# Optimization experiments

Measured on AMD Instinct MI355X. Metric: run time of the kernel, lower is better.

Reference implementation:

```python
import jax, jax.numpy as jnp
import numpy as np

NEG_BIG = -9e15
ALPHA = 0.1  # leaky relu slope


def setup_inputs() -> dict:
    key = jax.random.key(0)
    k1, k2, k3, k4 = jax.random.split(key, 4)
    B, C, N, F = 4, 4, 2048, 64
    x = jax.random.normal(k1, (B, C, N, F), dtype=jnp.float32)
    adj = jax.random.randint(k2, (N, N), 0, 2, dtype=jnp.int32)
    # xavier_uniform on shape (1,1,F,1): fan_in=1, fan_out=F -> bound = 1.414*sqrt(6/(1+F))
    bound = 1.414 * np.sqrt(6.0 / (1.0 + F))
    a1 = jax.random.uniform(k3, (F, 1), jnp.float32, -bound, bound)
    a2 = jax.random.uniform(k4, (F, 1), jnp.float32, -bound, bound)
    return {"x": x, "adj": adj, "a1": a1, "a2": a2}


def reference(x, adj, a1, a2):
    # x: [B, C, N, F]; adj: [N, N]; a1, a2: [F, 1]
    h = x
    f1 = jnp.einsum("bcnf,fo->bcn", h, a1)  # [B, C, N]
    f2 = jnp.einsum("bcnf,fo->bcn", h, a2)  # [B, C, N]
    e = f1[..., :, None] + f2[..., None, :]  # [B, C, N, N] additive scores
    e = jnp.where(e > 0, e, ALPHA * e)       # leaky relu
    e = jnp.where(adj[None, None] > 0, e, jnp.float32(NEG_BIG))
    attention = jax.nn.softmax(e, axis=-1)
    # dropout is identity in eval mode (training=False)
    return jnp.matmul(attention, h)          # [B, C, N, F]
```

## Files before the change

### kernel.cpp

```cpp
#include <hip/hip_runtime.h>
#include <hip/hip_bf16.h>
#include <cstdint>

#define NN 2048
#define FF 64
#define BCC 16

typedef float f32x4 __attribute__((ext_vector_type(4)));
typedef _Float16 half8 __attribute__((ext_vector_type(8)));
typedef uint32_t u32x4 __attribute__((ext_vector_type(4)));


__global__ __launch_bounds__(256) void k_prep(const float* __restrict__ x,
        const int* __restrict__ adj,
        const float* __restrict__ a1, const float* __restrict__ a2,
        _Float16* __restrict__ xP, _Float16* __restrict__ Uh,
        _Float16* __restrict__ Vh, _Float16* __restrict__ CIh,
        unsigned char* __restrict__ ADJP) {
    int tid = threadIdx.x;

    if (blockIdx.x >= 1024) {
        int wid  = tid >> 6;
        int lane = tid & 63;
        int idx = (blockIdx.x - 1024) * 4 + wid;
        int row = idx >> 3, cg = idx & 7;
        const int* p = adj + (size_t)row * NN + cg * 256 + lane;
        unsigned long long m0 = __ballot(p[0]   > 0);
        unsigned long long m1 = __ballot(p[64]  > 0);
        unsigned long long m2 = __ballot(p[128] > 0);
        unsigned long long m3 = __ballot(p[192] > 0);
        if (lane < 32) {
            int q = lane >> 3, s = lane & 7;
            unsigned long long m = (q == 0) ? m0 : (q == 1) ? m1
                                 : (q == 2) ? m2 : m3;
            unsigned char byte = (unsigned char)(m >> (8 * s));
            int jt = (cg * 4 + q) * 2 + (s >> 2);
            int g  = s & 3;
            ADJP[(size_t)row * 256 + g * 64 + jt] = byte;
        }
        return;
    }

    __shared__ float tile[32][65];
    __shared__ float red[2][32][8];
    int bc = blockIdx.x >> 6;
    int n0 = (blockIdx.x & 63) * 32;
    int row = tid >> 3;
    int fo  = (tid & 7) * 8;

    const float* xr = x + ((size_t)bc * NN + n0 + row) * FF + fo;
    f32x4 v0 = *(const f32x4*)xr;
    f32x4 v1 = *(const f32x4*)(xr + 4);
    *(f32x4*)&tile[row][fo]     = v0;
    *(f32x4*)&tile[row][fo + 4] = v1;

    f32x4 a1v0 = *(const f32x4*)(a1 + fo);
    f32x4 a1v1 = *(const f32x4*)(a1 + fo + 4);
    f32x4 a2v0 = *(const f32x4*)(a2 + fo);
    f32x4 a2v1 = *(const f32x4*)(a2 + fo + 4);
    float d1 = 0.f, d2 = 0.f;
    #pragma unroll
    for (int e = 0; e < 4; e++) {
        d1 += v0[e] * a1v0[e] + v1[e] * a1v1[e];
        d2 += v0[e] * a2v0[e] + v1[e] * a2v1[e];
    }
    red[0][row][tid & 7] = d1;
    red[1][row][tid & 7] = d2;
    __syncthreads();

    {
        int nb = tid >> 6, lane = tid & 63;
        int g = lane >> 4, l15 = lane & 15;
        half8 val;
        #pragma unroll
        for (int e = 0; e < 8; e++)
            val[e] = (_Float16)tile[8 * g + e][nb * 16 + l15];
        ((half8*)xP)[(((size_t)bc * 64 + (n0 >> 5)) * 4 + nb) * 64 + lane] = val;
    }
    if (tid < 32) {
        float f1 = 0.f, f2 = 0.f;
        #pragma unroll
        for (int s = 0; s < 8; s++) { f1 += red[0][tid][s]; f2 += red[1][tid][s]; }
        int idx = bc * NN + n0 + tid;
        Uh[idx]  = (_Float16)expf(f2);
        Vh[idx]  = (_Float16)expf(0.1f * f2);
        CIh[idx] = (_Float16)expf(-0.9f * f1);
    }
}

__global__ __launch_bounds__(256) void k_main(
        const _Float16* __restrict__ xP, const _Float16* __restrict__ Uh,
        const _Float16* __restrict__ Vh, const _Float16* __restrict__ CIh,
        const unsigned char* __restrict__ ADJP, float* __restrict__ out) {
    __shared__ _Float16 su[2048];
    __shared__ _Float16 sv[2048];
    __shared__ u32x4 lut[256];
    __shared__ float part[4][16][68];
    __shared__ float zp[4][16];

    int tid = threadIdx.x;
    int jq = tid >> 6, lane = tid & 63;
    int l15 = lane & 15, g = lane >> 4;

    int xcd = blockIdx.x & 7, kk = blockIdx.x >> 3;
    int bc   = (xcd << 1) | (kk >> 5);
    int iblk = kk & 31;
    int i0   = iblk * 64;

    ((u32x4*)su)[tid] = ((const u32x4*)(Uh + bc * NN))[tid];
    ((u32x4*)sv)[tid] = ((const u32x4*)(Vh + bc * NN))[tid];
    {
        uint32_t bb = tid;
        u32x4 lv;
        #pragma unroll
        for (int w = 0; w < 4; w++)
            lv[w] = (((bb >> (2 * w)) & 1u) ? 0xFFFFu : 0u)
                  | (((bb >> (2 * w + 1)) & 1u) ? 0xFFFF0000u : 0u);
        lut[bb] = lv;
    }
    const unsigned char* ab = ADJP + g * 64 + jq * 16;
    u32x4 adjw0 = *(const u32x4*)(ab + (size_t)(i0 + l15) * 256);
    u32x4 adjw1 = *(const u32x4*)(ab + (size_t)(i0 + 16 + l15) * 256);
    u32x4 adjw2 = *(const u32x4*)(ab + (size_t)(i0 + 32 + l15) * 256);
    u32x4 adjw3 = *(const u32x4*)(ab + (size_t)(i0 + 48 + l15) * 256);
    _Float16 Ci0 = CIh[bc * NN + i0 + l15];
    _Float16 Ci1 = CIh[bc * NN + i0 + 16 + l15];
    _Float16 Ci2 = CIh[bc * NN + i0 + 32 + l15];
    _Float16 Ci3 = CIh[bc * NN + i0 + 48 + l15];
    __syncthreads();

    f32x4 acc[4][4];
    #pragma unroll
    for (int a = 0; a < 4; a++)
        #pragma unroll
        for (int nb = 0; nb < 4; nb++)
            acc[a][nb] = (f32x4){0.f, 0.f, 0.f, 0.f};
    f32x4 accz[4];
    #pragma unroll
    for (int a = 0; a < 4; a++) accz[a] = (f32x4){0.f, 0.f, 0.f, 0.f};
    half8 onesh;
    #pragma unroll
    for (int e = 0; e < 8; e++) onesh[e] = (_Float16)1.0f;

    const u32x4* xPbc = (const u32x4*)xP + (size_t)bc * 16384;

    u32x4 A_x0, A_x1, A_x2, A_x3, B_x0, B_x1, B_x2, B_x3;

#define LOADX(P, J) do {                                                      \
        const u32x4* xw_ = xPbc + (((size_t)(jq * 16 + (J))) << 8) + lane;    \
        P##x0 = xw_[0]; P##x1 = xw_[64]; P##x2 = xw_[128]; P##x3 = xw_[192];  \
    } while (0)

#define GEN(AF, ADJW, CI) do {                                                \
        uint32_t b_ = (ADJW[(J_) >> 2] >> (((J_) & 3) * 8)) & 0xffu;          \
        u32x4 mm_ = lut[b_];                                                  \
        half8 mx_ = __builtin_elementwise_max(uu_, vv_ * (CI));               \
        AF = __builtin_bit_cast(half8, __builtin_bit_cast(u32x4, mx_) & mm_); \
    } while (0)

#define COMP(P, J) do {                                                       \
        const int J_ = (J);                                                   \
        const int jo_ = (jq * 16 + J_) * 32 + 8 * g;                          \
        half8 uu_ = *(const half8*)&su[jo_];                                  \
        half8 vv_ = *(const half8*)&sv[jo_];                                  \
        half8 af0_, af1_, af2_, af3_;                                         \
        GEN(af0_, adjw0, Ci0); GEN(af1_, adjw1, Ci1);                         \
        GEN(af2_, adjw2, Ci2); GEN(af3_, adjw3, Ci3);                         \
        half8 b0_ = __builtin_bit_cast(half8, P##x0);                         \
        half8 b1_ = __builtin_bit_cast(half8, P##x1);                         \
        half8 b2_ = __builtin_bit_cast(half8, P##x2);                         \
        half8 b3_ = __builtin_bit_cast(half8, P##x3);                         \
        __builtin_amdgcn_s_setprio(1);                                        \
        acc[0][0] = __builtin_amdgcn_mfma_f32_16x16x32_f16(af0_, b0_, acc[0][0], 0, 0, 0); \
        acc[0][1] = __builtin_amdgcn_mfma_f32_16x16x32_f16(af0_, b1_, acc[0][1], 0, 0, 0); \
        acc[0][2] = __builtin_amdgcn_mfma_f32_16x16x32_f16(af0_, b2_, acc[0][2], 0, 0, 0); \
        acc[0][3] = __builtin_amdgcn_mfma_f32_16x16x32_f16(af0_, b3_, acc[0][3], 0, 0, 0); \
        accz[0]   = __builtin_amdgcn_mfma_f32_16x16x32_f16(af0_, onesh, accz[0], 0, 0, 0); \
        acc[1][0] = __builtin_amdgcn_mfma_f32_16x16x32_f16(af1_, b0_, acc[1][0], 0, 0, 0); \
        acc[1][1] = __builtin_amdgcn_mfma_f32_16x16x32_f16(af1_, b1_, acc[1][1], 0, 0, 0); \
        acc[1][2] = __builtin_amdgcn_mfma_f32_16x16x32_f16(af1_, b2_, acc[1][2], 0, 0, 0); \
        acc[1][3] = __builtin_amdgcn_mfma_f32_16x16x32_f16(af1_, b3_, acc[1][3], 0, 0, 0); \
        accz[1]   = __builtin_amdgcn_mfma_f32_16x16x32_f16(af1_, onesh, accz[1], 0, 0, 0); \
        acc[2][0] = __builtin_amdgcn_mfma_f32_16x16x32_f16(af2_, b0_, acc[2][0], 0, 0, 0); \
        acc[2][1] = __builtin_amdgcn_mfma_f32_16x16x32_f16(af2_, b1_, acc[2][1], 0, 0, 0); \
        acc[2][2] = __builtin_amdgcn_mfma_f32_16x16x32_f16(af2_, b2_, acc[2][2], 0, 0, 0); \
        acc[2][3] = __builtin_amdgcn_mfma_f32_16x16x32_f16(af2_, b3_, acc[2][3], 0, 0, 0); \
        accz[2]   = __builtin_amdgcn_mfma_f32_16x16x32_f16(af2_, onesh, accz[2], 0, 0, 0); \
        acc[3][0] = __builtin_amdgcn_mfma_f32_16x16x32_f16(af3_, b0_, acc[3][0], 0, 0, 0); \
        acc[3][1] = __builtin_amdgcn_mfma_f32_16x16x32_f16(af3_, b1_, acc[3][1], 0, 0, 0); \
        acc[3][2] = __builtin_amdgcn_mfma_f32_16x16x32_f16(af3_, b2_, acc[3][2], 0, 0, 0); \
        acc[3][3] = __builtin_amdgcn_mfma_f32_16x16x32_f16(af3_, b3_, acc[3][3], 0, 0, 0); \
        accz[3]   = __builtin_amdgcn_mfma_f32_16x16x32_f16(af3_, onesh, accz[3], 0, 0, 0); \
        __builtin_amdgcn_s_setprio(0);                                        \
    } while (0)

    LOADX(A_, 0);
    LOADX(B_, 1);  COMP(A_, 0);
    LOADX(A_, 2);  COMP(B_, 1);
    LOADX(B_, 3);  COMP(A_, 2);
    LOADX(A_, 4);  COMP(B_, 3);
    LOADX(B_, 5);  COMP(A_, 4);
    LOADX(A_, 6);  COMP(B_, 5);
    LOADX(B_, 7);  COMP(A_, 6);
    LOADX(A_, 8);  COMP(B_, 7);
    LOADX(B_, 9);  COMP(A_, 8);
    LOADX(A_, 10); COMP(B_, 9);
    LOADX(B_, 11); COMP(A_, 10);
    LOADX(A_, 12); COMP(B_, 11);
    LOADX(B_, 13); COMP(A_, 12);
    LOADX(A_, 14); COMP(B_, 13);
    LOADX(B_, 15); COMP(A_, 14);
    COMP(B_, 15);
#undef LOADX
#undef GEN
#undef COMP

    float* outp = out + ((size_t)bc * NN + i0) * FF;
    #pragma unroll
    for (int a = 0; a < 4; a++) {
        #pragma unroll
        for (int nb = 0; nb < 4; nb++)
            #pragma unroll
            for (int r = 0; r < 4; r++)
                part[jq][4 * g + r][nb * 16 + l15] = acc[a][nb][r];
        if (l15 == 0) {
            #pragma unroll
            for (int r = 0; r < 4; r++)
                zp[jq][4 * g + r] = accz[a][r];
        }
        __syncthreads();
        #pragma unroll
        for (int rr = 0; rr < 4; rr++) {
            int row = jq * 4 + rr;
            float s = part[0][row][lane] + part[1][row][lane]
                    + part[2][row][lane] + part[3][row][lane];
            float z = zp[0][row] + zp[1][row] + zp[2][row] + zp[3][row];
            outp[(size_t)(16 * a + row) * FF + lane] = s / z;
        }
        __syncthreads();
    }
}

extern "C" void kernel_launch(void* const* d_in, const int* in_sizes, int n_in,
                              void* d_out, int out_size, void* d_ws, size_t ws_size,
                              hipStream_t stream) {
    const float* x  = (const float*)d_in[0];
    const int* adj  = (const int*)d_in[1];
    const float* a1 = (const float*)d_in[2];
    const float* a2 = (const float*)d_in[3];
    float* out = (float*)d_out;

    char* ws = (char*)d_ws;
    _Float16* xP  = (_Float16*)ws;
    _Float16* Uh  = (_Float16*)(ws + 4194304);
    _Float16* Vh  = (_Float16*)(ws + 4259840);
    _Float16* CIh = (_Float16*)(ws + 4325376);
    unsigned char* ADJP = (unsigned char*)(ws + 4390912);

    k_prep<<<1024 + 4096, 256, 0, stream>>>(x, adj, a1, a2, xP, Uh, Vh, CIh, ADJP);
    k_main<<<512, 256, 0, stream>>>(xP, Uh, Vh, CIh, ADJP, out);
}
```

Baseline: 25.93 us.

## Merge prep work into 512 blocks and pack adjacency with vector loads

Shrinks the prep grid from thousands of blocks to 512. Each block now processes two x tiles and then packs four adjacency rows. Adjacency bits are built per thread from 16-byte vector loads instead of wave ballots, which cuts block-launch overhead and the instruction count per byte. The risk is less memory-level parallelism and latency hiding, since there are far fewer waves in flight on a bandwidth-bound prep stage.

```diff
diff --git a/kernel.cpp b/kernel.cpp
--- a/kernel.cpp
+++ b/kernel.cpp
@@ -7,6 +7,7 @@
 #define BCC 16
 
 typedef float f32x4 __attribute__((ext_vector_type(4)));
+typedef int   i32x4 __attribute__((ext_vector_type(4)));
 typedef _Float16 half8 __attribute__((ext_vector_type(8)));
 typedef uint32_t u32x4 __attribute__((ext_vector_type(4)));
 
@@ -17,74 +18,78 @@
         _Float16* __restrict__ xP, _Float16* __restrict__ Uh,
         _Float16* __restrict__ Vh, _Float16* __restrict__ CIh,
         unsigned char* __restrict__ ADJP) {
-    int tid = threadIdx.x;
-
-    if (blockIdx.x >= 1024) {
-        int wid  = tid >> 6;
-        int lane = tid & 63;
-        int idx = (blockIdx.x - 1024) * 4 + wid;
-        int row = idx >> 3, cg = idx & 7;
-        const int* p = adj + (size_t)row * NN + cg * 256 + lane;
-        unsigned long long m0 = __ballot(p[0]   > 0);
-        unsigned long long m1 = __ballot(p[64]  > 0);
-        unsigned long long m2 = __ballot(p[128] > 0);
-        unsigned long long m3 = __ballot(p[192] > 0);
-        if (lane < 32) {
-            int q = lane >> 3, s = lane & 7;
-            unsigned long long m = (q == 0) ? m0 : (q == 1) ? m1
-                                 : (q == 2) ? m2 : m3;
-            unsigned char byte = (unsigned char)(m >> (8 * s));
-            int jt = (cg * 4 + q) * 2 + (s >> 2);
-            int g  = s & 3;
-            ADJP[(size_t)row * 256 + g * 64 + jt] = byte;
-        }
-        return;
-    }
-
     __shared__ float tile[32][65];
     __shared__ float red[2][32][8];
-    int bc = blockIdx.x >> 6;
-    int n0 = (blockIdx.x & 63) * 32;
-    int row = tid >> 3;
-    int fo  = (tid & 7) * 8;
-
-    const float* xr = x + ((size_t)bc * NN + n0 + row) * FF + fo;
-    f32x4 v0 = *(const f32x4*)xr;
-    f32x4 v1 = *(const f32x4*)(xr + 4);
-    *(f32x4*)&tile[row][fo]     = v0;
-    *(f32x4*)&tile[row][fo + 4] = v1;
-
-    f32x4 a1v0 = *(const f32x4*)(a1 + fo);
-    f32x4 a1v1 = *(const f32x4*)(a1 + fo + 4);
-    f32x4 a2v0 = *(const f32x4*)(a2 + fo);
-    f32x4 a2v1 = *(const f32x4*)(a2 + fo + 4);
-    float d1 = 0.f, d2 = 0.f;
-    #pragma unroll
-    for (int e = 0; e < 4; e++) {
-        d1 += v0[e] * a1v0[e] + v1[e] * a1v1[e];
-        d2 += v0[e] * a2v0[e] + v1[e] * a2v1[e];
-    }
-    red[0][row][tid & 7] = d1;
-    red[1][row][tid & 7] = d2;
-    __syncthreads();
+    int tid = threadIdx.x;
+
+    #pragma unroll
+    for (int tt = 0; tt < 2; tt++) {
+        int t  = blockIdx.x * 2 + tt;
+        int bc = t >> 6;
+        int n0 = (t & 63) * 32;
+        int row = tid >> 3;
+        int fo  = (tid & 7) * 8;
+
+        const float* xr = x + ((size_t)bc * NN + n0 + row) * FF + fo;
+        f32x4 v0 = *(const f32x4*)xr;
+        f32x4 v1 = *(const f32x4*)(xr + 4);
+        *(f32x4*)&tile[row][fo]     = v0;
+        *(f32x4*)&tile[row][fo + 4] = v1;
+
+        f32x4 a1v0 = *(const f32x4*)(a1 + fo);
+        f32x4 a1v1 = *(const f32x4*)(a1 + fo + 4);
+        f32x4 a2v0 = *(const f32x4*)(a2 + fo);
+        f32x4 a2v1 = *(const f32x4*)(a2 + fo + 4);
+        float d1 = 0.f, d2 = 0.f;
+        #pragma unroll
+        for (int e = 0; e < 4; e++) {
+            d1 += v0[e] * a1v0[e] + v1[e] * a1v1[e];
+            d2 += v0[e] * a2v0[e] + v1[e] * a2v1[e];
+        }
+        red[0][row][tid & 7] = d1;
+        red[1][row][tid & 7] = d2;
+        __syncthreads();
+
+        {
+            int nb = tid >> 6, lane = tid & 63;
+            int g = lane >> 4, l15 = lane & 15;
+            half8 val;
+            #pragma unroll
+            for (int e = 0; e < 8; e++)
+                val[e] = (_Float16)tile[8 * g + e][nb * 16 + l15];
+            ((half8*)xP)[(((size_t)bc * 64 + (n0 >> 5)) * 4 + nb) * 64 + lane] = val;
+        }
+        if (tid < 32) {
+            float f1 = 0.f, f2 = 0.f;
+            #pragma unroll
+            for (int s = 0; s < 8; s++) { f1 += red[0][tid][s]; f2 += red[1][tid][s]; }
+            int idx = bc * NN + n0 + tid;
+            Uh[idx]  = (_Float16)expf(f2);
+            Vh[idx]  = (_Float16)expf(0.1f * f2);
+            CIh[idx] = (_Float16)expf(-0.9f * f1);
+        }
+        __syncthreads();
+    }
 
     {
-        int nb = tid >> 6, lane = tid & 63;
-        int g = lane >> 4, l15 = lane & 15;
-        half8 val;
-        #pragma unroll
-        for (int e = 0; e < 8; e++)
-            val[e] = (_Float16)tile[8 * g + e][nb * 16 + l15];
-        ((half8*)xP)[(((size_t)bc * 64 + (n0 >> 5)) * 4 + nb) * 64 + lane] = val;
-    }
-    if (tid < 32) {
-        float f1 = 0.f, f2 = 0.f;
-        #pragma unroll
-        for (int s = 0; s < 8; s++) { f1 += red[0][tid][s]; f2 += red[1][tid][s]; }
-        int idx = bc * NN + n0 + tid;
-        Uh[idx]  = (_Float16)expf(f2);
-        Vh[idx]  = (_Float16)expf(0.1f * f2);
-        CIh[idx] = (_Float16)expf(-0.9f * f1);
+        int wid  = tid >> 6, lane = tid & 63;
+        int row  = blockIdx.x * 4 + wid;
+        const int* ar = adj + (size_t)row * NN;
+        unsigned char* ap = ADJP + (size_t)row * 256;
+        #pragma unroll
+        for (int m = 0; m < 4; m++) {
+            int o = lane + 64 * m;
+            const int* pj = ar + 8 * o;
+            i32x4 w0 = *(const i32x4*)pj;
+            i32x4 w1 = *(const i32x4*)(pj + 4);
+            uint32_t b = 0;
+            #pragma unroll
+            for (int e = 0; e < 4; e++) {
+                b |= (w0[e] > 0 ? 1u : 0u) << e;
+                b |= (w1[e] > 0 ? 1u : 0u) << (e + 4);
+            }
+            ap[(o & 3) * 64 + (o >> 2)] = (unsigned char)b;
+        }
     }
 }
 
@@ -257,6 +262,6 @@
     _Float16* CIh = (_Float16*)(ws + 4325376);
     unsigned char* ADJP = (unsigned char*)(ws + 4390912);
 
-    k_prep<<<1024 + 4096, 256, 0, stream>>>(x, adj, a1, a2, xP, Uh, Vh, CIh, ADJP);
+    k_prep<<<512, 256, 0, stream>>>(x, adj, a1, a2, xP, Uh, Vh, CIh, ADJP);
     k_main<<<512, 256, 0, stream>>>(xP, Uh, Vh, CIh, ADJP, out);
 }
```

After: 25.98 us. About the same (+0.2%).
